# Kernel optimization log

Hardware: AMD Instinct MI355X
Metric: run time of the kernel (lower is better)

Reference implementation:

```python
import jax, jax.numpy as jnp
import numpy as np
import math

LMAX = 2            # input lmax
LMAX_OUT = 2 * LMAX # gaunt product output lmax
RES_BETA = 20
RES_ALPHA = 39
N = 2048
MUL = 64
C = 64
BRANCHES = [(1, 1), (1, -1), (-1, 1)]  # (p_val1, p_val2) per branch


def _real_sh_grid(lmax, res_beta, res_alpha):
    """Real orthonormal spherical harmonics on a Gauss-Legendre x uniform-alpha grid.
    Returns Y [(lmax+1)^2, res_beta, res_alpha] and quadrature weights qw [res_beta]
    (beta GL weight times 2*pi/res_alpha alpha weight)."""
    x, w = np.polynomial.legendre.leggauss(res_beta)  # x = cos(beta)
    phi = np.linspace(0.0, 2.0 * np.pi, res_alpha, endpoint=False)
    # associated Legendre P[l, m] on x via standard recurrences
    P = np.zeros((lmax + 1, lmax + 1, res_beta))
    P[0, 0] = 1.0
    s = np.sqrt(1.0 - x ** 2)
    for m in range(1, lmax + 1):
        P[m, m] = -(2 * m - 1) * s * P[m - 1, m - 1]
    for m in range(lmax):
        P[m + 1, m] = (2 * m + 1) * x * P[m, m]
    for m in range(lmax + 1):
        for l in range(m + 2, lmax + 1):
            P[l, m] = ((2 * l - 1) * x * P[l - 1, m] - (l + m - 1) * P[l - 2, m]) / (l - m)
    Y = np.zeros(((lmax + 1) ** 2, res_beta, res_alpha))
    idx = 0
    for l in range(lmax + 1):
        for m in range(-l, l + 1):
            am = abs(m)
            K = math.sqrt((2 * l + 1) / (4 * math.pi) * math.factorial(l - am) / math.factorial(l + am))
            if m == 0:
                ang = np.ones(res_alpha)
            elif m > 0:
                ang = math.sqrt(2.0) * np.cos(m * phi)
            else:
                ang = math.sqrt(2.0) * np.sin(am * phi)
            Y[idx] = K * P[l, am][:, None] * ang[None, :]
            idx += 1
    qw = w * (2.0 * np.pi / res_alpha)
    return Y.astype(np.float32), qw.astype(np.float32)


def setup_inputs() -> dict:
    key = jax.random.key(0)
    k1, k2, k3, k4, k5 = jax.random.split(key, 5)
    # inputs carry both parities per l: [N, mul, parity(2), (lmax+1)^2]
    x1 = jax.random.normal(k1, (N, MUL, 2, (LMAX + 1) ** 2), dtype=jnp.float32)
    x2 = jax.random.normal(k2, (N, MUL, 2, (LMAX + 1) ** 2), dtype=jnp.float32)
    # per-branch, per-l linear weights (e3nn Linear mixes multiplicities within each irrep)
    W1 = jax.random.normal(k3, (3, LMAX + 1, MUL, C), dtype=jnp.float32)
    W2 = jax.random.normal(k4, (3, LMAX + 1, MUL, C), dtype=jnp.float32)
    Wout = jax.random.normal(k5, (3, LMAX_OUT + 1, C, C), dtype=jnp.float32)
    Yfull, qw = _real_sh_grid(LMAX_OUT, RES_BETA, RES_ALPHA)
    Y_in = jnp.asarray(Yfull[: (LMAX + 1) ** 2])   # [9, B, A]
    Y_out = jnp.asarray(Yfull)                     # [25, B, A]
    return {"x1": x1, "x2": x2, "W1": W1, "W2": W2, "Wout": Wout,
            "Y_in": Y_in, "Y_out": Y_out, "qw": jnp.asarray(qw)}


def _project(x, W, p_val):
    """e3nn Linear to s2_irreps(LMAX, p_val)*C: for each l, take the input block with
    parity p_val*(-1)^l and mix multiplicities. x [N,mul,2,L2], W [L, mul, C] -> [N, C, L2]."""
    blocks = []
    inv_sqrt_mul = 1.0 / np.sqrt(x.shape[1])
    for l in range(LMAX + 1):
        pidx = 0 if p_val * ((-1) ** l) == 1 else 1  # 0 = even, 1 = odd parity slot
        sl = slice(l * l, (l + 1) * (l + 1))
        blocks.append(jnp.einsum('nmk,mc->nck', x[:, :, pidx, sl], W[l]) * inv_sqrt_mul)
    return jnp.concatenate(blocks, axis=-1)  # [N, C, (LMAX+1)^2]


def _gaunt_branch(x1, x2, W1b, W2b, Woutb, p1, p2, Y_in, Y_out, qw):
    c1 = _project(x1, W1b, p1)                      # [N, C, 9]
    c2 = _project(x2, W2b, p2)
    # SH -> grid (inverse spherical transform)
    s1 = jnp.einsum('ncl,lba->ncba', c1, Y_in)      # [N, C, B, A]
    s2 = jnp.einsum('ncl,lba->ncba', c2, Y_in)
    # pointwise multiply on S2, then grid -> SH (forward transform w/ quadrature)
    co = jnp.einsum('ncba,lba,b->ncl', s1 * s2, Y_out, qw)  # [N, C, 25]
    # linear_out: per-l [C -> C] mixing
    inv_sqrt_c = 1.0 / np.sqrt(co.shape[1])
    outs = []
    for l in range(LMAX_OUT + 1):
        sl = slice(l * l, (l + 1) * (l + 1))
        outs.append(jnp.einsum('nck,cd->ndk', co[:, :, sl], Woutb[l]) * inv_sqrt_c)
    return jnp.concatenate(outs, axis=-1)           # [N, C, 25]


def reference(x1, x2, W1, W2, Wout, Y_in, Y_out, qw):
    outs = [_gaunt_branch(x1, x2, W1[b], W2[b], Wout[b], p1, p2, Y_in, Y_out, qw)
            for b, (p1, p2) in enumerate(BRANCHES)]
    return jnp.stack(outs, axis=1)                  # [N, 3, C, 25] (concat over parities)
```

## Files before the change

### kernel.cpp

```cpp
#include <hip/hip_runtime.h>
#include <utility>


#define NN 2048

__host__ __device__ constexpr int l_of9(int i)  { return i < 1 ? 0 : (i < 4 ? 1 : 2); }
__host__ __device__ constexpr int l_of25(int k) { return k < 1 ? 0 : (k < 4 ? 1 : (k < 9 ? 2 : (k < 16 ? 3 : 4))); }
__host__ __device__ constexpr int iabs_(int v)  { return v < 0 ? -v : v; }

__host__ __device__ constexpr bool gmask(int k, int i, int j) {
    const int l3 = l_of25(k), m3 = k - l3 * l3 - l3;
    const int l1 = l_of9(i),  m1 = i - l1 * l1 - l1;
    const int l2 = l_of9(j),  m2 = j - l2 * l2 - l2;
    if (((l1 + l2 + l3) & 1) != 0) return false;
    if (l3 > l1 + l2 || l3 < iabs_(l1 - l2)) return false;
    const int am3 = iabs_(m3);
    return (am3 == iabs_(m1 + m2)) || (am3 == iabs_(m1 - m2));
}

struct GTab {
    int po[82];
    int pc[81];
    int kl[81][12];
    constexpr GTab() : po{}, pc{}, kl{} {
        int off = 0;
        for (int ij = 0; ij < 81; ++ij) {
            po[ij] = off;
            const int i = ij / 9, j = ij % 9;
            int cnum = 0;
            for (int k = 0; k < 25; ++k)
                if (gmask(k, i, j)) kl[ij][cnum++] = k;
            pc[ij] = cnum;
            off += (cnum + 3) & ~3;
        }
        po[81] = off;
    }
};
constexpr GTab GT{};

__global__ __launch_bounds__(256) void gaunt_pack_kernel(
    const float* __restrict__ Y_in, const float* __restrict__ Y_out,
    const float* __restrict__ qw, float* __restrict__ gp)
{
    const int ij = blockIdx.x;
    const int i = ij / 9, j = ij % 9;
    const int t = threadIdx.x;

    __shared__ float yy[780];
    __shared__ float ps[25][8];
    __shared__ float gr[25];

    for (int p = t; p < 780; p += 256)
        yy[p] = Y_in[i * 780 + p] * Y_in[j * 780 + p] * qw[p / 39];
    __syncthreads();

    if (t < 200) {
        const int k = t >> 3, s = t & 7;
        const float* yo = Y_out + k * 780;
        const int p1 = (s * 98 + 98 < 780) ? (s * 98 + 98) : 780;
        float a = 0.f;
        for (int p = s * 98; p < p1; ++p) a = fmaf(yy[p], yo[p], a);
        ps[k][s] = a;
    }
    __syncthreads();

    if (t < 25) {
        float a = 0.f;
#pragma unroll
        for (int s = 0; s < 8; ++s) a += ps[t][s];
        gr[t] = a;
    }
    __syncthreads();

    const int cntp = (GT.pc[ij] + 3) & ~3;
    if (t < cntp)
        gp[GT.po[ij] + t] = (t < GT.pc[ij]) ? gr[GT.kl[ij][t]] : 0.f;
}

template <int IJ, int... Ts>
__device__ __forceinline__ void gaunt_apply(const float (&g)[12], float pij,
    float (&cov)[25], std::integer_sequence<int, Ts...>)
{
    ((cov[GT.kl[IJ][Ts]] = fmaf(g[Ts], pij, cov[GT.kl[IJ][Ts]])), ...);
}

template <int IJ>
__device__ __forceinline__ void gaunt_pair(const float* __restrict__ gp,
    const float (&c1)[9], const float (&c2)[9], float (&cov)[25])
{
    constexpr int cnt = GT.pc[IJ];
    if constexpr (cnt > 0) {
        constexpr int base = GT.po[IJ];
        constexpr int nv = (cnt + 3) / 4;
        const float pij = c1[IJ / 9] * c2[IJ % 9];
        float g[12];
#pragma unroll
        for (int q = 0; q < nv; ++q) {
            const float4 v = ((const float4*)(gp + base))[q];
            g[4 * q] = v.x; g[4 * q + 1] = v.y; g[4 * q + 2] = v.z; g[4 * q + 3] = v.w;
        }
        gaunt_apply<IJ>(g, pij, cov, std::make_integer_sequence<int, cnt>{});
    }
}

template <int I, int... Js>
__device__ __forceinline__ void gaunt_row(const float* __restrict__ gp,
    const float (&c1)[9], const float (&c2)[9], float (&cov)[25],
    std::integer_sequence<int, Js...>)
{
    (gaunt_pair<I * 9 + Js>(gp, c1, c2, cov), ...);
    __builtin_amdgcn_sched_barrier(0);
}

template <int... Is>
__device__ __forceinline__ void gaunt_all(const float* __restrict__ gp,
    const float (&c1)[9], const float (&c2)[9], float (&cov)[25],
    std::integer_sequence<int, Is...>)
{
    (gaunt_row<Is>(gp, c1, c2, cov, std::make_integer_sequence<int, 9>{}), ...);
}

template <int E1, int E2>
__device__ __forceinline__ void fused_body(
    const float* __restrict__ x1, const float* __restrict__ x2,
    const float* __restrict__ W1, const float* __restrict__ W2,
    const float* __restrict__ gp, float* __restrict__ out, int b)
{
    const int t = threadIdx.x;
    const int c = t & 63;
    const int w = __builtin_amdgcn_readfirstlane(t >> 6);
    const int n = blockIdx.x * 4 + w;

    const float* x1n = x1 + (size_t)n * 1152;
    const float* x2n = x2 + (size_t)n * 1152;
    const float* W1b = W1 + (size_t)b * 3 * 4096 + c;
    const float* W2b = W2 + (size_t)b * 3 * 4096 + c;

    float a1[9] = {0,0,0,0,0,0,0,0,0};
    float a2[9] = {0,0,0,0,0,0,0,0,0};

#pragma unroll 1
    for (int mp = 0; mp < 32; ++mp) {
        const float4* p1 = (const float4*)(x1n + mp * 36);
        const float4* p2 = (const float4*)(x2n + mp * 36);
        float xs1[36], xs2[36];
#pragma unroll
        for (int q = 0; q < 9; ++q) {
            const float4 t1 = p1[q], t2 = p2[q];
            xs1[4*q] = t1.x; xs1[4*q+1] = t1.y; xs1[4*q+2] = t1.z; xs1[4*q+3] = t1.w;
            xs2[4*q] = t2.x; xs2[4*q+1] = t2.y; xs2[4*q+2] = t2.z; xs2[4*q+3] = t2.w;
        }
        float w1v[3][2], w2v[3][2];
#pragma unroll
        for (int l = 0; l < 3; ++l)
#pragma unroll
            for (int mi = 0; mi < 2; ++mi) {
                const int moff = (l * 64 + mp * 2 + mi) * 64;
                w1v[l][mi] = W1b[moff];
                w2v[l][mi] = W2b[moff];
            }
#pragma unroll
        for (int l = 0; l < 3; ++l) {
            const int O1 = ((l & 1) ^ E1) * 9 + l * l;
            const int O2 = ((l & 1) ^ E2) * 9 + l * l;
#pragma unroll
            for (int mi = 0; mi < 2; ++mi)
#pragma unroll
                for (int ii = 0; ii <= 2 * l; ++ii) {
                    a1[l*l+ii] = fmaf(xs1[O1 + 18*mi + ii], w1v[l][mi], a1[l*l+ii]);
                    a2[l*l+ii] = fmaf(xs2[O2 + 18*mi + ii], w2v[l][mi], a2[l*l+ii]);
                }
        }
    }

    float c1[9], c2[9];
#pragma unroll
    for (int i = 0; i < 9; ++i) { c1[i] = a1[i] * 0.125f; c2[i] = a2[i] * 0.125f; }

    float cov[25] = {0,0,0,0,0,0,0,0,0,0,0,0,0,0,0,0,0,0,0,0,0,0,0,0,0};
    gaunt_all(gp, c1, c2, cov, std::make_integer_sequence<int, 9>{});

    float* cob = out + ((size_t)n * 3 + b) * 1600 + c;
#pragma unroll
    for (int k = 0; k < 25; ++k) cob[k * 64] = cov[k];
}

__global__ __launch_bounds__(256, 6) void fused_kernel(
    const float* __restrict__ x1, const float* __restrict__ x2,
    const float* __restrict__ W1, const float* __restrict__ W2,
    const float* __restrict__ gp, float* __restrict__ out)
{
    const int b = blockIdx.y;
    if (b == 0)      fused_body<0, 0>(x1, x2, W1, W2, gp, out, 0);
    else if (b == 1) fused_body<0, 1>(x1, x2, W1, W2, gp, out, 1);
    else             fused_body<1, 0>(x1, x2, W1, W2, gp, out, 2);
}

__global__ __launch_bounds__(64, 6) void mix_kernel(
    const float* __restrict__ Wout, float* __restrict__ io)
{
    const int n = blockIdx.x;
    const int b = blockIdx.y;
    const int c = threadIdx.x;

    __shared__ float st[1600];

    const float* cob = io + ((size_t)n * 3 + b) * 1600;
    const float* WoB = Wout + (size_t)b * 5 * 4096 + c;

    float acc[25];
#pragma unroll
    for (int k = 0; k < 25; ++k) acc[k] = 0.f;

#pragma unroll 1
    for (int dc = 0; dc < 16; ++dc) {
        const int d0 = dc * 4;
        float wr[5][4];
#pragma unroll
        for (int l3 = 0; l3 < 5; ++l3)
#pragma unroll
            for (int q = 0; q < 4; ++q)
                wr[l3][q] = WoB[(size_t)(l3 * 64 + d0 + q) * 64];

#pragma unroll
        for (int kg = 0; kg < 5; ++kg) {
#pragma unroll
            for (int kk = 0; kk < 5; ++kk) {
                const int k = kg * 5 + kk;
                const int l3 = l_of25(k);
                const float4 cv = *(const float4*)(cob + k * 64 + d0);
                acc[k] = fmaf(cv.x, wr[l3][0], acc[k]);
                acc[k] = fmaf(cv.y, wr[l3][1], acc[k]);
                acc[k] = fmaf(cv.z, wr[l3][2], acc[k]);
                acc[k] = fmaf(cv.w, wr[l3][3], acc[k]);
            }
            __builtin_amdgcn_sched_barrier(0);
        }
    }

#pragma unroll
    for (int k = 0; k < 25; ++k) st[c * 25 + k] = acc[k] * 0.125f;
    __syncthreads();

    float* op = io + ((size_t)n * 3 + b) * 1600;
#pragma unroll
    for (int r = 0; r < 6; ++r) {
        const float4 v = *(const float4*)&st[(r * 64 + c) * 4];
        *(float4*)(op + (r * 64 + c) * 4) = v;
    }
    if (c < 16) {
        const float4 v = *(const float4*)&st[(384 + c) * 4];
        *(float4*)(op + (384 + c) * 4) = v;
    }
}

extern "C" void kernel_launch(void* const* d_in, const int* in_sizes, int n_in,
                              void* d_out, int out_size, void* d_ws, size_t ws_size,
                              hipStream_t stream) {
    const float* x1    = (const float*)d_in[0];
    const float* x2    = (const float*)d_in[1];
    const float* W1    = (const float*)d_in[2];
    const float* W2    = (const float*)d_in[3];
    const float* Wout  = (const float*)d_in[4];
    const float* Y_in  = (const float*)d_in[5];
    const float* Y_out = (const float*)d_in[6];
    const float* qw    = (const float*)d_in[7];
    float* outp = (float*)d_out;
    float* gp   = (float*)d_ws;

    gaunt_pack_kernel<<<81, 256, 0, stream>>>(Y_in, Y_out, qw, gp);
    fused_kernel<<<dim3(NN / 4, 3), 256, 0, stream>>>(x1, x2, W1, W2, gp, outp);
    mix_kernel<<<dim3(NN, 3), 64, 0, stream>>>(Wout, outp);
}
```

Baseline: 140.2 us.

## Process all three branches per block to reuse x loads, with double-buffered prefetch

Fuses the three parity branches into one block, so each x1/x2 row is read once and feeds all three projections instead of being reloaded by three separate blocks. The x loads are double-buffered across multiplicity pairs so the next pair's loads overlap the current FMAs. Launch bounds drop from 6 to 2 blocks per CU because of the larger register footprint (54 accumulators plus two buffered x tiles), and the grid shrinks to 512 blocks. This lowers occupancy and parallelism.

```diff
diff --git a/kernel.cpp b/kernel.cpp
--- a/kernel.cpp
+++ b/kernel.cpp
@@ -120,80 +120,103 @@
     (gaunt_row<Is>(gp, c1, c2, cov, std::make_integer_sequence<int, 9>{}), ...);
 }
 
+__device__ __forceinline__ void load_x9(const float4* __restrict__ p,
+                                        float4 (&v)[9])
+{
+#pragma unroll
+    for (int q = 0; q < 9; ++q) v[q] = p[q];
+}
+
 template <int E1, int E2>
-__device__ __forceinline__ void fused_body(
-    const float* __restrict__ x1, const float* __restrict__ x2,
-    const float* __restrict__ W1, const float* __restrict__ W2,
-    const float* __restrict__ gp, float* __restrict__ out, int b)
-{
-    const int t = threadIdx.x;
-    const int c = t & 63;
-    const int w = __builtin_amdgcn_readfirstlane(t >> 6);
-    const int n = blockIdx.x * 4 + w;
-
-    const float* x1n = x1 + (size_t)n * 1152;
-    const float* x2n = x2 + (size_t)n * 1152;
-    const float* W1b = W1 + (size_t)b * 3 * 4096 + c;
-    const float* W2b = W2 + (size_t)b * 3 * 4096 + c;
-
-    float a1[9] = {0,0,0,0,0,0,0,0,0};
-    float a2[9] = {0,0,0,0,0,0,0,0,0};
-
-#pragma unroll 1
-    for (int mp = 0; mp < 32; ++mp) {
-        const float4* p1 = (const float4*)(x1n + mp * 36);
-        const float4* p2 = (const float4*)(x2n + mp * 36);
-        float xs1[36], xs2[36];
-#pragma unroll
-        for (int q = 0; q < 9; ++q) {
-            const float4 t1 = p1[q], t2 = p2[q];
-            xs1[4*q] = t1.x; xs1[4*q+1] = t1.y; xs1[4*q+2] = t1.z; xs1[4*q+3] = t1.w;
-            xs2[4*q] = t2.x; xs2[4*q+1] = t2.y; xs2[4*q+2] = t2.z; xs2[4*q+3] = t2.w;
-        }
-        float w1v[3][2], w2v[3][2];
-#pragma unroll
-        for (int l = 0; l < 3; ++l)
-#pragma unroll
-            for (int mi = 0; mi < 2; ++mi) {
-                const int moff = (l * 64 + mp * 2 + mi) * 64;
-                w1v[l][mi] = W1b[moff];
-                w2v[l][mi] = W2b[moff];
+__device__ __forceinline__ void proj_step(const float (&xs1)[36],
+    const float (&xs2)[36], const float* __restrict__ W1p,
+    const float* __restrict__ W2p, float (&a1)[9], float (&a2)[9])
+{
+#pragma unroll
+    for (int l = 0; l < 3; ++l) {
+        const int O1 = ((l & 1) ^ E1) * 9 + l * l;
+        const int O2 = ((l & 1) ^ E2) * 9 + l * l;
+#pragma unroll
+        for (int mi = 0; mi < 2; ++mi) {
+            const float w1v = W1p[l * 4096 + mi * 64];
+            const float w2v = W2p[l * 4096 + mi * 64];
+#pragma unroll
+            for (int ii = 0; ii <= 2 * l; ++ii) {
+                a1[l*l+ii] = fmaf(xs1[O1 + 18*mi + ii], w1v, a1[l*l+ii]);
+                a2[l*l+ii] = fmaf(xs2[O2 + 18*mi + ii], w2v, a2[l*l+ii]);
             }
-#pragma unroll
-        for (int l = 0; l < 3; ++l) {
-            const int O1 = ((l & 1) ^ E1) * 9 + l * l;
-            const int O2 = ((l & 1) ^ E2) * 9 + l * l;
-#pragma unroll
-            for (int mi = 0; mi < 2; ++mi)
-#pragma unroll
-                for (int ii = 0; ii <= 2 * l; ++ii) {
-                    a1[l*l+ii] = fmaf(xs1[O1 + 18*mi + ii], w1v[l][mi], a1[l*l+ii]);
-                    a2[l*l+ii] = fmaf(xs2[O2 + 18*mi + ii], w2v[l][mi], a2[l*l+ii]);
-                }
-        }
-    }
-
-    float c1[9], c2[9];
-#pragma unroll
-    for (int i = 0; i < 9; ++i) { c1[i] = a1[i] * 0.125f; c2[i] = a2[i] * 0.125f; }
-
-    float cov[25] = {0,0,0,0,0,0,0,0,0,0,0,0,0,0,0,0,0,0,0,0,0,0,0,0,0};
-    gaunt_all(gp, c1, c2, cov, std::make_integer_sequence<int, 9>{});
-
-    float* cob = out + ((size_t)n * 3 + b) * 1600 + c;
-#pragma unroll
-    for (int k = 0; k < 25; ++k) cob[k * 64] = cov[k];
-}
-
-__global__ __launch_bounds__(256, 6) void fused_kernel(
+        }
+    }
+}
+
+__global__ __launch_bounds__(256, 2) void fused_kernel(
     const float* __restrict__ x1, const float* __restrict__ x2,
     const float* __restrict__ W1, const float* __restrict__ W2,
     const float* __restrict__ gp, float* __restrict__ out)
 {
-    const int b = blockIdx.y;
-    if (b == 0)      fused_body<0, 0>(x1, x2, W1, W2, gp, out, 0);
-    else if (b == 1) fused_body<0, 1>(x1, x2, W1, W2, gp, out, 1);
-    else             fused_body<1, 0>(x1, x2, W1, W2, gp, out, 2);
+    const int t = threadIdx.x;
+    const int c = t & 63;
+    const int w = t >> 6;
+    const int n = blockIdx.x * 4 + w;
+
+    const float4* px1 = (const float4*)(x1 + (size_t)n * 1152);
+    const float4* px2 = (const float4*)(x2 + (size_t)n * 1152);
+    const float* W1c = W1 + c;
+    const float* W2c = W2 + c;
+
+    float a1[3][9], a2[3][9];
+#pragma unroll
+    for (int b = 0; b < 3; ++b)
+#pragma unroll
+        for (int i = 0; i < 9; ++i) { a1[b][i] = 0.f; a2[b][i] = 0.f; }
+
+    float4 xA1[9], xA2[9], xB1[9], xB2[9];
+    load_x9(px1, xA1);
+    load_x9(px2, xA2);
+
+    auto do_pair = [&](const float4 (&v1)[9], const float4 (&v2)[9], int mp) {
+        float xs1[36], xs2[36];
+#pragma unroll
+        for (int q = 0; q < 9; ++q) {
+            xs1[4*q] = v1[q].x; xs1[4*q+1] = v1[q].y;
+            xs1[4*q+2] = v1[q].z; xs1[4*q+3] = v1[q].w;
+            xs2[4*q] = v2[q].x; xs2[4*q+1] = v2[q].y;
+            xs2[4*q+2] = v2[q].z; xs2[4*q+3] = v2[q].w;
+        }
+        const float* W1p = W1c + mp * 128;
+        const float* W2p = W2c + mp * 128;
+        proj_step<0, 0>(xs1, xs2, W1p,         W2p,         a1[0], a2[0]);
+        proj_step<0, 1>(xs1, xs2, W1p + 12288, W2p + 12288, a1[1], a2[1]);
+        proj_step<1, 0>(xs1, xs2, W1p + 24576, W2p + 24576, a1[2], a2[2]);
+    };
+
+#pragma unroll 1
+    for (int mp = 0; mp < 32; mp += 2) {
+        load_x9(px1 + (mp + 1) * 9, xB1);
+        load_x9(px2 + (mp + 1) * 9, xB2);
+        do_pair(xA1, xA2, mp);
+        if (mp + 2 < 32) {
+            load_x9(px1 + (mp + 2) * 9, xA1);
+            load_x9(px2 + (mp + 2) * 9, xA2);
+        }
+        do_pair(xB1, xB2, mp + 1);
+    }
+
+#pragma unroll
+    for (int b = 0; b < 3; ++b) {
+        float c1[9], c2[9];
+#pragma unroll
+        for (int i = 0; i < 9; ++i) {
+            c1[i] = a1[b][i] * 0.125f;
+            c2[i] = a2[b][i] * 0.125f;
+        }
+        float cov[25] = {0,0,0,0,0,0,0,0,0,0,0,0,0,0,0,0,0,0,0,0,0,0,0,0,0};
+        gaunt_all(gp, c1, c2, cov, std::make_integer_sequence<int, 9>{});
+
+        float* cob = out + ((size_t)n * 3 + b) * 1600 + c;
+#pragma unroll
+        for (int k = 0; k < 25; ++k) cob[k * 64] = cov[k];
+    }
 }
 
 __global__ __launch_bounds__(64, 6) void mix_kernel(
@@ -269,6 +292,6 @@
     float* gp   = (float*)d_ws;
 
     gaunt_pack_kernel<<<81, 256, 0, stream>>>(Y_in, Y_out, qw, gp);
-    fused_kernel<<<dim3(NN / 4, 3), 256, 0, stream>>>(x1, x2, W1, W2, gp, outp);
+    fused_kernel<<<NN / 4, 256, 0, stream>>>(x1, x2, W1, W2, gp, outp);
     mix_kernel<<<dim3(NN, 3), 64, 0, stream>>>(Wout, outp);
 }
```

Result: slower. 173.5 us (+23.8%).

## Remap projection threads to 8 nodes by 2 channels per thread

Applied to the files above, without the earlier changes.

The projection-plus-gaunt kernel now gives each thread one node and two output channels, with 8 nodes per block, instead of one node per wavefront and one channel per lane. Each x row loaded is reused for two channels, which halves the per-channel x loads, although lanes in a wave now read different node rows. The 1/8 * 1/8 scaling of c1*c2 is folded into the packed gaunt coefficients, which removes per-thread multiplies. Register pressure doubles, so the launch bound drops to 3 blocks per SM, and the W loads are now gathered across channels.

```diff
diff --git a/kernel.cpp b/kernel.cpp
--- a/kernel.cpp
+++ b/kernel.cpp
@@ -74,7 +74,7 @@
 
     const int cntp = (GT.pc[ij] + 3) & ~3;
     if (t < cntp)
-        gp[GT.po[ij] + t] = (t < GT.pc[ij]) ? gr[GT.kl[ij][t]] : 0.f;
+        gp[GT.po[ij] + t] = (t < GT.pc[ij]) ? gr[GT.kl[ij][t]] * 0.015625f : 0.f;
 }
 
 template <int IJ, int... Ts>
@@ -121,79 +121,103 @@
 }
 
 template <int E1, int E2>
-__device__ __forceinline__ void fused_body(
+__device__ __forceinline__ void k1_body(
     const float* __restrict__ x1, const float* __restrict__ x2,
     const float* __restrict__ W1, const float* __restrict__ W2,
     const float* __restrict__ gp, float* __restrict__ out, int b)
 {
-    const int t = threadIdx.x;
-    const int c = t & 63;
-    const int w = __builtin_amdgcn_readfirstlane(t >> 6);
-    const int n = blockIdx.x * 4 + w;
-
-    const float* x1n = x1 + (size_t)n * 1152;
-    const float* x2n = x2 + (size_t)n * 1152;
-    const float* W1b = W1 + (size_t)b * 3 * 4096 + c;
-    const float* W2b = W2 + (size_t)b * 3 * 4096 + c;
-
-    float a1[9] = {0,0,0,0,0,0,0,0,0};
-    float a2[9] = {0,0,0,0,0,0,0,0,0};
+    const int t   = threadIdx.x;
+    const int c_l = t & 7;
+    const int n_l = (t >> 3) & 7;
+    const int w   = t >> 6;
+    const int n   = blockIdx.x * 8 + n_l;
+
+    const float4* px1 = (const float4*)(x1 + (size_t)n * 1152);
+    const float4* px2 = (const float4*)(x2 + (size_t)n * 1152);
+    const float* W1a = W1 + (size_t)b * 12288;
+    const float* W2a = W2 + (size_t)b * 12288;
+    const int cc0 = w * 8 + c_l;
+    const int cc1 = cc0 + 32;
+
+    float a1[2][9], a2[2][9];
+#pragma unroll
+    for (int i = 0; i < 9; ++i) {
+        a1[0][i] = 0.f; a1[1][i] = 0.f;
+        a2[0][i] = 0.f; a2[1][i] = 0.f;
+    }
 
 #pragma unroll 1
     for (int mp = 0; mp < 32; ++mp) {
-        const float4* p1 = (const float4*)(x1n + mp * 36);
-        const float4* p2 = (const float4*)(x2n + mp * 36);
+        float4 v1[9], v2[9];
+#pragma unroll
+        for (int q = 0; q < 9; ++q) v1[q] = px1[mp * 9 + q];
+#pragma unroll
+        for (int q = 0; q < 9; ++q) v2[q] = px2[mp * 9 + q];
+
+        float w1r[2][3][2], w2r[2][3][2];
+#pragma unroll
+        for (int l = 0; l < 3; ++l)
+#pragma unroll
+            for (int mi = 0; mi < 2; ++mi) {
+                const int o = (l * 64 + mp * 2 + mi) * 64;
+                w1r[0][l][mi] = W1a[o + cc0];
+                w1r[1][l][mi] = W1a[o + cc1];
+                w2r[0][l][mi] = W2a[o + cc0];
+                w2r[1][l][mi] = W2a[o + cc1];
+            }
+
         float xs1[36], xs2[36];
 #pragma unroll
         for (int q = 0; q < 9; ++q) {
-            const float4 t1 = p1[q], t2 = p2[q];
-            xs1[4*q] = t1.x; xs1[4*q+1] = t1.y; xs1[4*q+2] = t1.z; xs1[4*q+3] = t1.w;
-            xs2[4*q] = t2.x; xs2[4*q+1] = t2.y; xs2[4*q+2] = t2.z; xs2[4*q+3] = t2.w;
-        }
-        float w1v[3][2], w2v[3][2];
-#pragma unroll
-        for (int l = 0; l < 3; ++l)
-#pragma unroll
-            for (int mi = 0; mi < 2; ++mi) {
-                const int moff = (l * 64 + mp * 2 + mi) * 64;
-                w1v[l][mi] = W1b[moff];
-                w2v[l][mi] = W2b[moff];
+            xs1[4*q] = v1[q].x; xs1[4*q+1] = v1[q].y;
+            xs1[4*q+2] = v1[q].z; xs1[4*q+3] = v1[q].w;
+            xs2[4*q] = v2[q].x; xs2[4*q+1] = v2[q].y;
+            xs2[4*q+2] = v2[q].z; xs2[4*q+3] = v2[q].w;
+        }
+
+#pragma unroll
+        for (int cg = 0; cg < 2; ++cg)
+#pragma unroll
+            for (int l = 0; l < 3; ++l) {
+                const int s1 = ((l & 1) ^ E1) * 9 + l * l;
+                const int s2 = ((l & 1) ^ E2) * 9 + l * l;
+#pragma unroll
+                for (int mi = 0; mi < 2; ++mi)
+#pragma unroll
+                    for (int ii = 0; ii <= 2 * l; ++ii) {
+                        a1[cg][l*l+ii] = fmaf(xs1[18*mi + s1 + ii],
+                                              w1r[cg][l][mi], a1[cg][l*l+ii]);
+                        a2[cg][l*l+ii] = fmaf(xs2[18*mi + s2 + ii],
+                                              w2r[cg][l][mi], a2[cg][l*l+ii]);
+                    }
             }
-#pragma unroll
-        for (int l = 0; l < 3; ++l) {
-            const int O1 = ((l & 1) ^ E1) * 9 + l * l;
-            const int O2 = ((l & 1) ^ E2) * 9 + l * l;
-#pragma unroll
-            for (int mi = 0; mi < 2; ++mi)
-#pragma unroll
-                for (int ii = 0; ii <= 2 * l; ++ii) {
-                    a1[l*l+ii] = fmaf(xs1[O1 + 18*mi + ii], w1v[l][mi], a1[l*l+ii]);
-                    a2[l*l+ii] = fmaf(xs2[O2 + 18*mi + ii], w2v[l][mi], a2[l*l+ii]);
-                }
-        }
-    }
-
-    float c1[9], c2[9];
-#pragma unroll
-    for (int i = 0; i < 9; ++i) { c1[i] = a1[i] * 0.125f; c2[i] = a2[i] * 0.125f; }
-
-    float cov[25] = {0,0,0,0,0,0,0,0,0,0,0,0,0,0,0,0,0,0,0,0,0,0,0,0,0};
-    gaunt_all(gp, c1, c2, cov, std::make_integer_sequence<int, 9>{});
-
-    float* cob = out + ((size_t)n * 3 + b) * 1600 + c;
-#pragma unroll
-    for (int k = 0; k < 25; ++k) cob[k * 64] = cov[k];
-}
-
-__global__ __launch_bounds__(256, 6) void fused_kernel(
+    }
+
+#pragma unroll
+    for (int cg = 0; cg < 2; ++cg) {
+        float c1[9], c2[9];
+#pragma unroll
+        for (int i = 0; i < 9; ++i) { c1[i] = a1[cg][i]; c2[i] = a2[cg][i]; }
+
+        float cov[25] = {0,0,0,0,0,0,0,0,0,0,0,0,0,0,0,0,0,0,0,0,0,0,0,0,0};
+        gaunt_all(gp, c1, c2, cov, std::make_integer_sequence<int, 9>{});
+
+        const int cc = cg ? cc1 : cc0;
+        float* cob = out + ((size_t)n * 3 + b) * 1600 + cc;
+#pragma unroll
+        for (int k = 0; k < 25; ++k) cob[k * 64] = cov[k];
+    }
+}
+
+__global__ __launch_bounds__(256, 3) void proj_gaunt_kernel(
     const float* __restrict__ x1, const float* __restrict__ x2,
     const float* __restrict__ W1, const float* __restrict__ W2,
     const float* __restrict__ gp, float* __restrict__ out)
 {
     const int b = blockIdx.y;
-    if (b == 0)      fused_body<0, 0>(x1, x2, W1, W2, gp, out, 0);
-    else if (b == 1) fused_body<0, 1>(x1, x2, W1, W2, gp, out, 1);
-    else             fused_body<1, 0>(x1, x2, W1, W2, gp, out, 2);
+    if (b == 0)      k1_body<0, 0>(x1, x2, W1, W2, gp, out, 0);
+    else if (b == 1) k1_body<0, 1>(x1, x2, W1, W2, gp, out, 1);
+    else             k1_body<1, 0>(x1, x2, W1, W2, gp, out, 2);
 }
 
 __global__ __launch_bounds__(64, 6) void mix_kernel(
@@ -269,6 +293,6 @@
     float* gp   = (float*)d_ws;
 
     gaunt_pack_kernel<<<81, 256, 0, stream>>>(Y_in, Y_out, qw, gp);
-    fused_kernel<<<dim3(NN / 4, 3), 256, 0, stream>>>(x1, x2, W1, W2, gp, outp);
+    proj_gaunt_kernel<<<dim3(NN / 8, 3), 256, 0, stream>>>(x1, x2, W1, W2, gp, outp);
     mix_kernel<<<dim3(NN, 3), 64, 0, stream>>>(Wout, outp);
 }
```

Result: slower. 178.3 us (+27.2%).
